# Kernel tuning notes

Hardware: AMD Instinct MI355X
Metric: run time of the kernel (lower is better)

## Reference

```python
import jax, jax.numpy as jnp
import numpy as np

N_NODES = 100000
N_EDGES = 1600000
IN_FEATS = 128
HIDDEN = 128


def _graph_conv(x, W, b, src, dst, n_nodes):
    # DGL GraphConv with norm='both': out = D_in^{-1/2} * A^T * (D_out^{-1/2} * x) @ W + b
    ones = jnp.ones((src.shape[0],), dtype=x.dtype)
    deg_out = jax.ops.segment_sum(ones, src, num_segments=n_nodes)
    deg_in = jax.ops.segment_sum(ones, dst, num_segments=n_nodes)
    norm_src = jax.lax.rsqrt(jnp.clip(deg_out, 1.0))  # [N]
    norm_dst = jax.lax.rsqrt(jnp.clip(deg_in, 1.0))   # [N]
    h = x @ W                                          # [N, F_out]
    msg = h[src] * norm_src[src][:, None]              # gather by edge src: [E, F_out]
    agg = jax.ops.segment_sum(msg, dst, num_segments=n_nodes)  # scatter-add to dst
    return agg * norm_dst[:, None] + b


def setup_inputs() -> dict:
    key = jax.random.key(0)
    ks = jax.random.split(key, 9)
    x = jax.random.normal(ks[0], (N_NODES, IN_FEATS), dtype=jnp.float32)
    src = jax.random.randint(ks[1], (N_EDGES,), 0, N_NODES, dtype=jnp.int32)
    dst = jax.random.randint(ks[2], (N_EDGES,), 0, N_NODES, dtype=jnp.int32)
    s1 = 1.0 / np.sqrt(IN_FEATS)
    s2 = 1.0 / np.sqrt(HIDDEN)
    W1 = jax.random.uniform(ks[3], (IN_FEATS, HIDDEN), jnp.float32, -s1, s1)
    b1 = jnp.zeros((HIDDEN,), jnp.float32)
    W2 = jax.random.uniform(ks[4], (HIDDEN, HIDDEN), jnp.float32, -s2, s2)
    b2 = jnp.zeros((HIDDEN,), jnp.float32)
    sp = 1.0 / np.sqrt(2 * HIDDEN)
    Wp = jax.random.uniform(ks[5], (2 * HIDDEN, 1), jnp.float32, -sp, sp)
    bp = jax.random.uniform(ks[6], (1,), jnp.float32, -sp, sp)
    return {"x": x, "W1": W1, "b1": b1, "W2": W2, "b2": b2,
            "Wp": Wp, "bp": bp, "src": src, "dst": dst}


def reference(x, W1, b1, W2, b2, Wp, bp, src, dst):
    n_nodes = x.shape[0]
    h = _graph_conv(x, W1, b1, src, dst, n_nodes)
    h = jax.nn.relu(h)
    h = _graph_conv(h, W2, b2, src, dst, n_nodes)  # final node embeddings [N, H]
    # predict_links on the same edge list: cat(h[u], h[v]) -> linear -> sigmoid
    edge_h = jnp.concatenate([h[src], h[dst]], axis=1)  # [E, 2H]
    scores = jax.nn.sigmoid(edge_h @ Wp + bp)           # [E, 1]
    return scores
```

## Files before the change

kernel.cpp:

```cpp
#include <hip/hip_runtime.h>
#include <cstdint>
#include <cstddef>

#define NN 100000
#define NE 1600000
#define F  128
#define NPAD 100352
#define NBUCK 782
#define BCAPG 2560
#define CHUNK 6250

__device__ __forceinline__ unsigned short f2bf(float f) {
    unsigned u = __float_as_uint(f);
    unsigned r = (u + 0x7fffu + ((u >> 16) & 1u)) >> 16;
    return (unsigned short)r;
}
__device__ __forceinline__ void acc_bf8s(const uint4 v, const float ns, float* acc) {
    acc[0] += __uint_as_float(v.x << 16) * ns;
    acc[1] += __uint_as_float(v.x & 0xffff0000u) * ns;
    acc[2] += __uint_as_float(v.y << 16) * ns;
    acc[3] += __uint_as_float(v.y & 0xffff0000u) * ns;
    acc[4] += __uint_as_float(v.z << 16) * ns;
    acc[5] += __uint_as_float(v.z & 0xffff0000u) * ns;
    acc[6] += __uint_as_float(v.w << 16) * ns;
    acc[7] += __uint_as_float(v.w & 0xffff0000u) * ns;
}

__global__ void head_const_kernel(const float* __restrict__ b2, const float* __restrict__ Wp,
                                  const float* __restrict__ bp, float* __restrict__ consts) {
    const int l = threadIdx.x;
    const float2 bb = *(const float2*)&b2[2 * l];
    const float2 wa = *(const float2*)&Wp[2 * l];
    const float2 wc = *(const float2*)&Wp[F + 2 * l];
    float s = bb.x * (wa.x + wc.x) + bb.y * (wa.y + wc.y);
    #pragma unroll
    for (int m = 32; m > 0; m >>= 1) s += __shfl_xor(s, m);
    if (l == 0) consts[0] = s + bp[0];
}

__global__ void headw_kernel(const float* __restrict__ W2, const float* __restrict__ Wp,
                             float2* __restrict__ V) {
    const int i = threadIdx.x;
    float sa = 0.f, sc = 0.f;
    #pragma unroll 8
    for (int j = 0; j < F; ++j) {
        const float w = W2[i * F + j];
        sa += w * Wp[j];
        sc += w * Wp[F + j];
    }
    V[i] = make_float2(sa, sc);
}

__global__ void init_cursor_kernel(int* __restrict__ gCur) {
    const int b = blockIdx.x * blockDim.x + threadIdx.x;
    if (b < NBUCK) gCur[b] = b * BCAPG;
}

__global__ __launch_bounds__(256, 2)
void gemm1_fill_kernel(const float* __restrict__ in, const float* __restrict__ W,
                       unsigned short* __restrict__ out_bf,
                       const int* __restrict__ src, const int* __restrict__ dst,
                       int* __restrict__ deg_out, int* __restrict__ gCur,
                       int* __restrict__ srcPart) {
    __shared__ __align__(16) float Ws[F * F];
    __shared__ __align__(16) float xs[32][F];

    const int g = blockIdx.x;
    const int r3 = g % 3;
    const int tid = threadIdx.x;

    if (r3 == 2) {
        int* packedL = (int*)Ws;
        unsigned short* bktL = (unsigned short*)(packedL + CHUNK);
        int* hist = (int*)(bktL + CHUNK);
        int* curL = hist + NBUCK;
        const int e0 = (g / 3) * CHUNK;
        const int nCh = min(CHUNK, NE - e0);
        for (int i = tid; i < NBUCK; i += 256) hist[i] = 0;
        __syncthreads();
        for (int i = tid; i < nCh; i += 256) {
            const int s = src[e0 + i];
            const int d = dst[e0 + i];
            atomicAdd(&deg_out[s], 1);
            const int bkt = d >> 7;
            atomicAdd(&hist[bkt], 1);
            packedL[i] = s | ((d & 127) << 17);
            bktL[i] = (unsigned short)bkt;
        }
        __syncthreads();
        for (int b = tid; b < NBUCK; b += 256) {
            const int c = hist[b];
            curL[b] = (c > 0) ? atomicAdd(&gCur[b], c) : 0;
        }
        __syncthreads();
        for (int i = tid; i < nCh; i += 256) {
            const int bkt = bktL[i];
            const int p = atomicAdd(&curL[bkt], 1);
            if (p < (bkt + 1) * BCAPG)
                srcPart[p] = packedL[i];
        }
        return;
    }

    const int gid = (g / 3) * 2 + r3;
    for (int i = tid * 4; i < F * F; i += 256 * 4) {
        *(float4*)&Ws[i] = *(const float4*)&W[i];
    }

    const int l  = tid & 63;
    const int w  = tid >> 6;
    const int cg = l & 31;
    const int rg = l >> 5;
    const int c0 = cg * 4;

    const int nTiles = NN / 32;
    for (int tile = gid; tile < nTiles; tile += 512) {
        const int row0 = tile * 32;
        __syncthreads();
        for (int i = tid; i < 32 * 32; i += 256) {
            const int r  = i >> 5;
            const int k4 = (i & 31) * 4;
            *(float4*)&xs[r][k4] = *(const float4*)&in[(size_t)(row0 + r) * F + k4];
        }
        __syncthreads();

        const int r0 = 8 * w + 4 * rg;
        float4 a0 = {0,0,0,0}, a1 = {0,0,0,0}, a2 = {0,0,0,0}, a3 = {0,0,0,0};
        #pragma unroll 8
        for (int k = 0; k < F; ++k) {
            const float4 wv = *(const float4*)&Ws[k * F + c0];
            const float x0 = xs[r0 + 0][k];
            const float x1 = xs[r0 + 1][k];
            const float x2 = xs[r0 + 2][k];
            const float x3 = xs[r0 + 3][k];
            a0.x += x0 * wv.x; a0.y += x0 * wv.y; a0.z += x0 * wv.z; a0.w += x0 * wv.w;
            a1.x += x1 * wv.x; a1.y += x1 * wv.y; a1.z += x1 * wv.z; a1.w += x1 * wv.w;
            a2.x += x2 * wv.x; a2.y += x2 * wv.y; a2.z += x2 * wv.z; a2.w += x2 * wv.w;
            a3.x += x3 * wv.x; a3.y += x3 * wv.y; a3.z += x3 * wv.z; a3.w += x3 * wv.w;
        }
        ushort4 o;
        o.x = f2bf(a0.x); o.y = f2bf(a0.y); o.z = f2bf(a0.z); o.w = f2bf(a0.w);
        *(ushort4*)&out_bf[(size_t)(row0 + r0 + 0) * F + c0] = o;
        o.x = f2bf(a1.x); o.y = f2bf(a1.y); o.z = f2bf(a1.z); o.w = f2bf(a1.w);
        *(ushort4*)&out_bf[(size_t)(row0 + r0 + 1) * F + c0] = o;
        o.x = f2bf(a2.x); o.y = f2bf(a2.y); o.z = f2bf(a2.z); o.w = f2bf(a2.w);
        *(ushort4*)&out_bf[(size_t)(row0 + r0 + 2) * F + c0] = o;
        o.x = f2bf(a3.x); o.y = f2bf(a3.y); o.z = f2bf(a3.z); o.w = f2bf(a3.w);
        *(ushort4*)&out_bf[(size_t)(row0 + r0 + 3) * F + c0] = o;
    }
}

__global__ void normsrc_kernel(const int* __restrict__ deg_out, float* __restrict__ norm_src, int nN) {
    const int n = blockIdx.x * blockDim.x + threadIdx.x;
    if (n < nN) norm_src[n] = rsqrtf((float)max(deg_out[n], 1));
}

__global__ __launch_bounds__(256)
void gather_sort_kernel(const unsigned short* __restrict__ hs,
                        int* __restrict__ srcPart, const int* __restrict__ gCur,
                        const float* __restrict__ norm_src, const float* __restrict__ bias,
                        const float2* __restrict__ V, float2* __restrict__ uw,
                        int* __restrict__ offs, int* __restrict__ ends,
                        float* __restrict__ norm_dst) {
    __shared__ int cnt[128];
    __shared__ int loc[128];
    __shared__ int cur[128];
    __shared__ int sortedL[BCAPG];

    const int b   = blockIdx.x;
    const int tid = threadIdx.x;
    const int nlo = b * 128;
    const int nCnt = min(128, NN - nlo);
    const int eBase = b * BCAPG;
    const int total = min(gCur[b] - eBase, BCAPG);

    if (tid < 128) cnt[tid] = 0;
    __syncthreads();
    for (int i = tid; i < total; i += 256)
        atomicAdd(&cnt[(srcPart[eBase + i] >> 17) & 127], 1);
    __syncthreads();
    if (tid < 128) loc[tid] = cnt[tid];
    __syncthreads();
    for (int off = 1; off < 128; off <<= 1) {
        int v = 0;
        if (tid < 128 && tid >= off) v = loc[tid - off];
        __syncthreads();
        if (tid < 128) loc[tid] += v;
        __syncthreads();
    }
    if (tid < 128) cur[tid] = loc[tid] - cnt[tid];
    if (tid < nCnt) {
        const int st = eBase + loc[tid] - cnt[tid];
        offs[nlo + tid] = st;
        ends[nlo + tid] = st + cnt[tid];
        norm_dst[nlo + tid] = rsqrtf((float)max(cnt[tid], 1));
    }
    __syncthreads();
    for (int i = tid; i < total; i += 256) {
        const int v = srcPart[eBase + i];
        const int r = atomicAdd(&cur[(v >> 17) & 127], 1);
        sortedL[r] = v & 0x1FFFF;
    }
    __syncthreads();
    for (int i = tid; i < total; i += 256)
        srcPart[eBase + i] = sortedL[i];

    const int w  = tid >> 6;
    const int l  = tid & 63;
    const int q  = l >> 4;
    const int c8 = (l & 15) * 8;
    float bb[8];
    *(float4*)&bb[0] = *(const float4*)&bias[c8];
    *(float4*)&bb[4] = *(const float4*)&bias[c8 + 4];
    float2 Vl[8];
    #pragma unroll
    for (int k = 0; k < 8; ++k) Vl[k] = V[c8 + k];

    const int nhEnd = min((w + 1) * 32, nCnt);
    for (int nh = w * 32; nh < nhEnd; ++nh) {
        const int end = loc[nh];
        const int beg = end - cnt[nh];
        float acc[8] = {0.f, 0.f, 0.f, 0.f, 0.f, 0.f, 0.f, 0.f};
        int j = beg;
        for (; j + 8 <= end; j += 8) {
            const int s0 = sortedL[j + q];
            const int s1 = sortedL[j + 4 + q];
            const float ns0 = norm_src[s0];
            const float ns1 = norm_src[s1];
            const uint4 v0 = *(const uint4*)&hs[(size_t)s0 * F + c8];
            const uint4 v1 = *(const uint4*)&hs[(size_t)s1 * F + c8];
            acc_bf8s(v0, ns0, acc);
            acc_bf8s(v1, ns1, acc);
        }
        for (; j + 4 <= end; j += 4) {
            const int s = sortedL[j + q];
            const float ns = norm_src[s];
            const uint4 v = *(const uint4*)&hs[(size_t)s * F + c8];
            acc_bf8s(v, ns, acc);
        }
        if (j + q < end) {
            const int s = sortedL[j + q];
            const float ns = norm_src[s];
            const uint4 v = *(const uint4*)&hs[(size_t)s * F + c8];
            acc_bf8s(v, ns, acc);
        }
        #pragma unroll
        for (int k = 0; k < 8; ++k) {
            acc[k] += __shfl_xor(acc[k], 16);
            acc[k] += __shfl_xor(acc[k], 32);
        }

        const int n = nlo + nh;
        const float nd = rsqrtf((float)max(cnt[nh], 1));
        float pa = 0.f, pc = 0.f;
        #pragma unroll
        for (int k = 0; k < 8; ++k) {
            const float ok = fmaxf(acc[k] * nd + bb[k], 0.f);
            pa += ok * Vl[k].x;
            pc += ok * Vl[k].y;
        }
        #pragma unroll
        for (int m = 1; m <= 8; m <<= 1) {
            pa += __shfl_xor(pa, m);
            pc += __shfl_xor(pc, m);
        }
        if (l == 0) {
            const float ns = norm_src[n];
            uw[n] = make_float2(ns * pa, ns * pc);
        }
    }
}

__global__ void ac_kernel(const float2* __restrict__ uw, const int* __restrict__ sorted_src,
                          const int* __restrict__ offs, const int* __restrict__ ends,
                          const float* __restrict__ norm_dst,
                          float* __restrict__ A, float* __restrict__ C, int nN) {
    const int n = blockIdx.x * blockDim.x + threadIdx.x;
    if (n >= nN) return;
    const int beg = offs[n];
    const int end = ends[n];
    float su = 0.f, sw = 0.f;
    int j = beg;
    for (; j + 2 <= end; j += 2) {
        const float2 t0 = uw[sorted_src[j]];
        const float2 t1 = uw[sorted_src[j + 1]];
        su += t0.x + t1.x;
        sw += t0.y + t1.y;
    }
    if (j < end) {
        const float2 t = uw[sorted_src[j]];
        su += t.x;
        sw += t.y;
    }
    const float nd = norm_dst[n];
    A[n] = nd * su;
    C[n] = nd * sw;
}

__global__ void score_kernel(const float* __restrict__ A, const float* __restrict__ C,
                             const int* __restrict__ src, const int* __restrict__ dst,
                             const float* __restrict__ consts, float* __restrict__ out, int nE) {
    const int e = blockIdx.x * blockDim.x + threadIdx.x;
    if (e < nE) {
        const float z = A[src[e]] + C[dst[e]] + consts[0];
        out[e] = 1.f / (1.f + __expf(-z));
    }
}

extern "C" void kernel_launch(void* const* d_in, const int* in_sizes, int n_in,
                              void* d_out, int out_size, void* d_ws, size_t ws_size,
                              hipStream_t stream) {
    const float* x  = (const float*)d_in[0];
    const float* W1 = (const float*)d_in[1];
    const float* b1 = (const float*)d_in[2];
    const float* W2 = (const float*)d_in[3];
    const float* b2 = (const float*)d_in[4];
    const float* Wp = (const float*)d_in[5];
    const float* bp = (const float*)d_in[6];
    const int*   src = (const int*)d_in[7];
    const int*   dst = (const int*)d_in[8];
    float* out = (float*)d_out;

    float* ws        = (float*)d_ws;
    float* norm_src  = ws;
    float* bufA      = ws + NPAD;
    float* bufC      = ws + 2 * NPAD;
    float* norm_dst  = ws + 3 * NPAD;
    int*   offs      = (int*)(ws + 4 * NPAD);
    int*   ends      = offs + NPAD;
    int*   gCur      = ends + NPAD;
    float* consts    = (float*)(gCur + 1024);
    float2* V        = (float2*)(consts + 16);
    float2* uw       = V + 128;
    int*   srcPart   = (int*)(uw + NN);
    unsigned short* hs_bf = (unsigned short*)(srcPart + NBUCK * BCAPG);

    hipMemsetAsync(bufA, 0, NPAD * sizeof(int), stream);
    init_cursor_kernel<<<4, 256, 0, stream>>>(gCur);
    head_const_kernel<<<1, 64, 0, stream>>>(b2, Wp, bp, consts);
    headw_kernel<<<1, 128, 0, stream>>>(W2, Wp, V);

    gemm1_fill_kernel<<<768, 256, 0, stream>>>(x, W1, hs_bf, src, dst,
                                               (int*)bufA, gCur, srcPart);

    normsrc_kernel<<<(NN + 255) / 256, 256, 0, stream>>>((const int*)bufA, norm_src, NN);

    gather_sort_kernel<<<NBUCK, 256, 0, stream>>>(hs_bf, srcPart, gCur, norm_src, b1,
                                                  V, uw, offs, ends, norm_dst);

    ac_kernel<<<(NN + 255) / 256, 256, 0, stream>>>(uw, srcPart, offs, ends, norm_dst,
                                                    bufA, bufC, NN);

    score_kernel<<<(NE + 255) / 256, 256, 0, stream>>>(bufA, bufC, src, dst, consts, out, NE);
}
```

Baseline: 331.1 us.

## Use split-bf16 MFMA for first GEMM and rebalance fill/GEMM blocks

Replaces the scalar fp32 FMA GEMM in the fused gemm1/fill kernel with MFMA 16x16x32 bf16 instructions. The input is split into hi and lo bf16 parts so accuracy stays close to fp32, and the weights are held as bf16 fragments in registers. Shared memory shrinks because W no longer sits in LDS, which allows occupancy 3 and an even split between fill and GEMM blocks with smaller edge chunks. The gather loop also gets a 16-edge unrolled step for more memory-level parallelism. The trade-offs are that W is rounded to bf16, which loses some precision, and output stores become scalar 2-byte writes.

```diff
diff --git a/kernel.cpp b/kernel.cpp
--- a/kernel.cpp
+++ b/kernel.cpp
@@ -8,7 +8,11 @@
 #define NPAD 100352
 #define NBUCK 782
 #define BCAPG 2560
-#define CHUNK 6250
+#define FILLB 384
+#define CHUNK 4167
+
+typedef __attribute__((ext_vector_type(8))) short bf16x8;
+typedef __attribute__((ext_vector_type(4))) float f32x4;
 
 __device__ __forceinline__ unsigned short f2bf(float f) {
     unsigned u = __float_as_uint(f);
@@ -56,25 +60,23 @@
     if (b < NBUCK) gCur[b] = b * BCAPG;
 }
 
-__global__ __launch_bounds__(256, 2)
+__global__ __launch_bounds__(256, 3)
 void gemm1_fill_kernel(const float* __restrict__ in, const float* __restrict__ W,
                        unsigned short* __restrict__ out_bf,
                        const int* __restrict__ src, const int* __restrict__ dst,
                        int* __restrict__ deg_out, int* __restrict__ gCur,
                        int* __restrict__ srcPart) {
-    __shared__ __align__(16) float Ws[F * F];
-    __shared__ __align__(16) float xs[32][F];
+    __shared__ __align__(16) char smem[31264];
 
     const int g = blockIdx.x;
-    const int r3 = g % 3;
     const int tid = threadIdx.x;
 
-    if (r3 == 2) {
-        int* packedL = (int*)Ws;
+    if (g & 1) {
+        int* packedL = (int*)smem;
         unsigned short* bktL = (unsigned short*)(packedL + CHUNK);
-        int* hist = (int*)(bktL + CHUNK);
+        int* hist = (int*)((char*)smem + 25008);
         int* curL = hist + NBUCK;
-        const int e0 = (g / 3) * CHUNK;
+        const int e0 = (g >> 1) * CHUNK;
         const int nCh = min(CHUNK, NE - e0);
         for (int i = tid; i < NBUCK; i += 256) hist[i] = 0;
         __syncthreads();
@@ -102,51 +104,87 @@
         return;
     }
 
-    const int gid = (g / 3) * 2 + r3;
-    for (int i = tid * 4; i < F * F; i += 256 * 4) {
-        *(float4*)&Ws[i] = *(const float4*)&W[i];
-    }
-
-    const int l  = tid & 63;
-    const int w  = tid >> 6;
-    const int cg = l & 31;
-    const int rg = l >> 5;
-    const int c0 = cg * 4;
+    char* A_hi = smem;
+    char* A_lo = smem + 8192;
+
+    const int gid  = g >> 1;
+    const int w    = tid >> 6;
+    const int lane = tid & 63;
+    const int ml   = lane & 15;
+    const int quad = lane >> 4;
+
+    bf16x8 Bf[4][2];
+    #pragma unroll
+    for (int kb = 0; kb < 4; ++kb) {
+        #pragma unroll
+        for (int nb = 0; nb < 2; ++nb) {
+            const int n = 32 * w + nb * 16 + ml;
+            const int k0 = kb * 32 + quad * 8;
+            #pragma unroll
+            for (int j = 0; j < 8; ++j)
+                Bf[kb][nb][j] = (short)f2bf(W[(k0 + j) * F + n]);
+        }
+    }
 
     const int nTiles = NN / 32;
-    for (int tile = gid; tile < nTiles; tile += 512) {
+    for (int tile = gid; tile < nTiles; tile += 384) {
         const int row0 = tile * 32;
         __syncthreads();
-        for (int i = tid; i < 32 * 32; i += 256) {
-            const int r  = i >> 5;
-            const int k4 = (i & 31) * 4;
-            *(float4*)&xs[r][k4] = *(const float4*)&in[(size_t)(row0 + r) * F + k4];
-        }
-        __syncthreads();
-
-        const int r0 = 8 * w + 4 * rg;
-        float4 a0 = {0,0,0,0}, a1 = {0,0,0,0}, a2 = {0,0,0,0}, a3 = {0,0,0,0};
-        #pragma unroll 8
-        for (int k = 0; k < F; ++k) {
-            const float4 wv = *(const float4*)&Ws[k * F + c0];
-            const float x0 = xs[r0 + 0][k];
-            const float x1 = xs[r0 + 1][k];
-            const float x2 = xs[r0 + 2][k];
-            const float x3 = xs[r0 + 3][k];
-            a0.x += x0 * wv.x; a0.y += x0 * wv.y; a0.z += x0 * wv.z; a0.w += x0 * wv.w;
-            a1.x += x1 * wv.x; a1.y += x1 * wv.y; a1.z += x1 * wv.z; a1.w += x1 * wv.w;
-            a2.x += x2 * wv.x; a2.y += x2 * wv.y; a2.z += x2 * wv.z; a2.w += x2 * wv.w;
-            a3.x += x3 * wv.x; a3.y += x3 * wv.y; a3.z += x3 * wv.z; a3.w += x3 * wv.w;
-        }
-        ushort4 o;
-        o.x = f2bf(a0.x); o.y = f2bf(a0.y); o.z = f2bf(a0.z); o.w = f2bf(a0.w);
-        *(ushort4*)&out_bf[(size_t)(row0 + r0 + 0) * F + c0] = o;
-        o.x = f2bf(a1.x); o.y = f2bf(a1.y); o.z = f2bf(a1.z); o.w = f2bf(a1.w);
-        *(ushort4*)&out_bf[(size_t)(row0 + r0 + 1) * F + c0] = o;
-        o.x = f2bf(a2.x); o.y = f2bf(a2.y); o.z = f2bf(a2.z); o.w = f2bf(a2.w);
-        *(ushort4*)&out_bf[(size_t)(row0 + r0 + 2) * F + c0] = o;
-        o.x = f2bf(a3.x); o.y = f2bf(a3.y); o.z = f2bf(a3.z); o.w = f2bf(a3.w);
-        *(ushort4*)&out_bf[(size_t)(row0 + r0 + 3) * F + c0] = o;
+        #pragma unroll
+        for (int c = 0; c < 2; ++c) {
+            const int i2 = tid + 256 * c;
+            const int m  = i2 >> 4;
+            const int o  = i2 & 15;
+            const float* xr = &in[(size_t)(row0 + m) * F + o * 8];
+            const float4 v0 = *(const float4*)xr;
+            const float4 v1 = *(const float4*)(xr + 4);
+            float xv[8] = {v0.x, v0.y, v0.z, v0.w, v1.x, v1.y, v1.z, v1.w};
+            short hi8[8], lo8[8];
+            #pragma unroll
+            for (int j = 0; j < 8; ++j) {
+                const unsigned short h = f2bf(xv[j]);
+                hi8[j] = (short)h;
+                lo8[j] = (short)f2bf(xv[j] - __uint_as_float((unsigned)h << 16));
+            }
+            const int kb2 = o >> 2, q2 = o & 3, ml2 = m & 15, mh2 = m >> 4;
+            const int fo = (((mh2 * 4 + kb2) * 64) + q2 * 16 + ml2) * 16;
+            *(bf16x8*)(A_hi + fo) = *(bf16x8*)hi8;
+            *(bf16x8*)(A_lo + fo) = *(bf16x8*)lo8;
+        }
+        __syncthreads();
+
+        f32x4 acc00 = {0,0,0,0}, acc01 = {0,0,0,0}, acc10 = {0,0,0,0}, acc11 = {0,0,0,0};
+        #pragma unroll
+        for (int kb = 0; kb < 4; ++kb) {
+            const int o0 = (kb * 64 + lane) * 16;
+            const int o1 = ((4 + kb) * 64 + lane) * 16;
+            const bf16x8 ah0 = *(const bf16x8*)(A_hi + o0);
+            const bf16x8 ah1 = *(const bf16x8*)(A_hi + o1);
+            const bf16x8 al0 = *(const bf16x8*)(A_lo + o0);
+            const bf16x8 al1 = *(const bf16x8*)(A_lo + o1);
+            acc00 = __builtin_amdgcn_mfma_f32_16x16x32_bf16(ah0, Bf[kb][0], acc00, 0, 0, 0);
+            acc00 = __builtin_amdgcn_mfma_f32_16x16x32_bf16(al0, Bf[kb][0], acc00, 0, 0, 0);
+            acc01 = __builtin_amdgcn_mfma_f32_16x16x32_bf16(ah0, Bf[kb][1], acc01, 0, 0, 0);
+            acc01 = __builtin_amdgcn_mfma_f32_16x16x32_bf16(al0, Bf[kb][1], acc01, 0, 0, 0);
+            acc10 = __builtin_amdgcn_mfma_f32_16x16x32_bf16(ah1, Bf[kb][0], acc10, 0, 0, 0);
+            acc10 = __builtin_amdgcn_mfma_f32_16x16x32_bf16(al1, Bf[kb][0], acc10, 0, 0, 0);
+            acc11 = __builtin_amdgcn_mfma_f32_16x16x32_bf16(ah1, Bf[kb][1], acc11, 0, 0, 0);
+            acc11 = __builtin_amdgcn_mfma_f32_16x16x32_bf16(al1, Bf[kb][1], acc11, 0, 0, 0);
+        }
+
+        #pragma unroll
+        for (int mh = 0; mh < 2; ++mh) {
+            #pragma unroll
+            for (int nb = 0; nb < 2; ++nb) {
+                const f32x4 a = (mh == 0) ? (nb == 0 ? acc00 : acc01)
+                                          : (nb == 0 ? acc10 : acc11);
+                const int row = row0 + mh * 16 + quad * 4;
+                const int col = 32 * w + nb * 16 + ml;
+                #pragma unroll
+                for (int r = 0; r < 4; ++r)
+                    out_bf[(size_t)(row + r) * F + col] = f2bf(a[r]);
+            }
+        }
     }
 }
 
@@ -222,6 +260,24 @@
         const int beg = end - cnt[nh];
         float acc[8] = {0.f, 0.f, 0.f, 0.f, 0.f, 0.f, 0.f, 0.f};
         int j = beg;
+        for (; j + 16 <= end; j += 16) {
+            const int s0 = sortedL[j + q];
+            const int s1 = sortedL[j + 4 + q];
+            const int s2 = sortedL[j + 8 + q];
+            const int s3 = sortedL[j + 12 + q];
+            const float ns0 = norm_src[s0];
+            const float ns1 = norm_src[s1];
+            const float ns2 = norm_src[s2];
+            const float ns3 = norm_src[s3];
+            const uint4 v0 = *(const uint4*)&hs[(size_t)s0 * F + c8];
+            const uint4 v1 = *(const uint4*)&hs[(size_t)s1 * F + c8];
+            const uint4 v2 = *(const uint4*)&hs[(size_t)s2 * F + c8];
+            const uint4 v3 = *(const uint4*)&hs[(size_t)s3 * F + c8];
+            acc_bf8s(v0, ns0, acc);
+            acc_bf8s(v1, ns1, acc);
+            acc_bf8s(v2, ns2, acc);
+            acc_bf8s(v3, ns3, acc);
+        }
         for (; j + 8 <= end; j += 8) {
             const int s0 = sortedL[j + q];
             const int s1 = sortedL[j + 4 + q];
```

Measured after the change: 314.8 us. 1.05x faster.
